# Kernel optimization log

Measured on AMD Instinct MI355X. Metric: run time of the kernel, lower is better.

## Reference

```python
import jax, jax.numpy as jnp
import numpy as np


def _three_nn(xyz1, xyz2):
    # xyz1: [B,N1,3], xyz2: [B,N2,3]
    # Squared euclidean distances, as in the original three_nn CUDA/TF op.
    d2 = (jnp.sum(xyz1 * xyz1, axis=-1)[:, :, None]
          + jnp.sum(xyz2 * xyz2, axis=-1)[:, None, :]
          - 2.0 * jnp.einsum('bnd,bmd->bnm', xyz1, xyz2))  # [B,N1,N2]
    neg_vals, idx = jax.lax.top_k(-d2, 3)                 # 3 smallest
    return -neg_vals, idx                                  # dist [B,N1,3], idx [B,N1,3]


def reference(xyz1, xyz2, points1, points2, w1, w2):
    dist, idx = _three_nn(xyz1, xyz2)
    dist = jnp.maximum(dist, 1e-10)
    inv = 1.0 / dist                                       # [B,N1,3]
    weight = inv / jnp.sum(inv, axis=2, keepdims=True)     # [B,N1,3]

    B = points2.shape[0]
    b_idx = jnp.arange(B)[:, None, None]
    gathered = points2[b_idx, idx]                         # [B,N1,3,C2]
    interpolated = jnp.einsum('bnk,bnkc->bnc', weight, gathered)  # [B,N1,C2]

    new_points = jnp.concatenate([interpolated, points1], axis=2)  # [B,N1,C2+C1]

    # 1x1 conv MLP = per-point matmul; bn=False, activation=relu on all layers
    h = jax.nn.relu(jnp.einsum('bnc,cf->bnf', new_points, w1))
    h = jax.nn.relu(jnp.einsum('bnc,cf->bnf', h, w2))
    return h


def setup_inputs() -> dict:
    key = jax.random.key(0)
    k1, k2, k3, k4, k5, k6 = jax.random.split(key, 6)
    B, N1, N2, C1, C2 = 4, 8192, 2048, 128, 256
    xyz1 = jax.random.normal(k1, (B, N1, 3), dtype=jnp.float32)
    xyz2 = jax.random.normal(k2, (B, N2, 3), dtype=jnp.float32)
    points1 = jax.random.normal(k3, (B, N1, C1), dtype=jnp.float32)
    points2 = jax.random.normal(k4, (B, N2, C2), dtype=jnp.float32)
    # glorot-normal-ish init for the 1x1 conv kernels
    w1 = jax.random.normal(k5, (C2 + C1, 256), dtype=jnp.float32) * (2.0 / (C2 + C1 + 256)) ** 0.5
    w2 = jax.random.normal(k6, (256, 256), dtype=jnp.float32) * (2.0 / (256 + 256)) ** 0.5
    return {"xyz1": xyz1, "xyz2": xyz2, "points1": points1, "points2": points2, "w1": w1, "w2": w2}
```

## Files before the change

### kernel.cpp

```cpp
#include <hip/hip_runtime.h>
#include <stdint.h>

typedef unsigned short u16;
typedef unsigned int   u32;

#define NB 4
#define N1 8192
#define N2 2048
#define C1 128
#define C2 256
#define KK1 384
#define FF 256
#define TM 64
#define NTHR 1024
#define NCH 16
#define PTSA 768
#define SUBA (PTSA / NCH)
#define PTSB 1280
#define SUBB (PTSB / NCH)
#define TILES_PER_B (N1 / TM)
#define APAD 400
#define HPAD 272
#define NKT1 (KK1 / 32)
#define NKT2 (FF / 32)

typedef short short8 __attribute__((ext_vector_type(8)));
typedef float floatx4 __attribute__((ext_vector_type(4)));
typedef float f32x2  __attribute__((ext_vector_type(2)));
typedef u32   u32x4  __attribute__((ext_vector_type(4)));

union ABFrag { u32 u[4]; short8 v; u32x4 q; };

__device__ __forceinline__ u16 f2b(float f) {
    u32 x = __float_as_uint(f);
    return (u16)((x + 0x7FFFu + ((x >> 16) & 1u)) >> 16);
}
__device__ __forceinline__ u32 pack2(float a, float b) {
    u32 r;
    asm("v_cvt_pk_bf16_f32 %0, %1, %2" : "=v"(r) : "v"(a), "v"(b));
    return r;
}

__global__ __launch_bounds__(256) void prep_kernel(
    const float* __restrict__ w1, const float* __restrict__ w2,
    const float* __restrict__ xyz2,
    u32x4* __restrict__ w1F, u32x4* __restrict__ w2F, float* __restrict__ xq)
{
    int i = blockIdx.x * 256 + threadIdx.x;
    if (i < 16 * NKT1 * 64) {
        int nt = i / (NKT1 * 64), rem = i % (NKT1 * 64);
        int kt = rem / 64, lane = rem % 64;
        int n  = nt * 16 + (lane & 15);
        int k0 = kt * 32 + (lane >> 4) * 8;
        const float* wc = w1 + n;
        ABFrag f;
        f.u[0] = pack2(wc[(k0 + 0) * FF], wc[(k0 + 1) * FF]);
        f.u[1] = pack2(wc[(k0 + 2) * FF], wc[(k0 + 3) * FF]);
        f.u[2] = pack2(wc[(k0 + 4) * FF], wc[(k0 + 5) * FF]);
        f.u[3] = pack2(wc[(k0 + 6) * FF], wc[(k0 + 7) * FF]);
        w1F[i] = f.q;
        return;
    }
    i -= 16 * NKT1 * 64;
    if (i < 16 * NKT2 * 64) {
        int nt = i / (NKT2 * 64), rem = i % (NKT2 * 64);
        int kt = rem / 64, lane = rem % 64;
        int n  = nt * 16 + (lane & 15);
        int k0 = kt * 32 + (lane >> 4) * 8;
        const float* wc = w2 + n;
        ABFrag f;
        f.u[0] = pack2(wc[(k0 + 0) * FF], wc[(k0 + 1) * FF]);
        f.u[1] = pack2(wc[(k0 + 2) * FF], wc[(k0 + 3) * FF]);
        f.u[2] = pack2(wc[(k0 + 4) * FF], wc[(k0 + 5) * FF]);
        f.u[3] = pack2(wc[(k0 + 6) * FF], wc[(k0 + 7) * FF]);
        w2F[i] = f.q;
        return;
    }
    i -= 16 * NKT2 * 64;
    if (i < NB * N2) {
        const float* q = xyz2 + (size_t)i * 3;
        float x = q[0], y = q[1], z = q[2];
        float s2 = __fadd_rn(__fadd_rn(__fmul_rn(x,x), __fmul_rn(y,y)), __fmul_rn(z,z));
        int p = i >> 1, e = i & 1;
        float* rec = xq + (size_t)p * 8;
        rec[0 + e] = -2.0f * x;
        rec[2 + e] = -2.0f * y;
        rec[4 + e] = -2.0f * z;
        rec[6 + e] = s2;
    }
}

__global__ __launch_bounds__(NTHR, 8) void fp_fused_kernel(
    const float* __restrict__ xyz1, const float* __restrict__ p1,
    const float* __restrict__ p2,
    const u32x4* __restrict__ w1F,  const u32x4* __restrict__ w2F,
    const float4* __restrict__ xq,  float* __restrict__ out)
{
    __shared__ int   s_idx[TM][3];
    __shared__ float s_wt[TM][3];
    __shared__ float s_m[TM][8];
    __shared__ float s_pd[NCH * TM * 3];
    __shared__ int   s_pi[NCH * TM * 3];
    __shared__ __align__(16) char s_buf[TM * APAD * 2];

    const int tid = threadIdx.x;
    const int b   = blockIdx.x / TILES_PER_B;
    const int t0  = (blockIdx.x % TILES_PER_B) * TM;
    u16* A = (u16*)s_buf;

    {
        const int c4 = (tid & 31) * 4, r32 = tid >> 5;
        #pragma unroll
        for (int rv = 0; rv < 2; ++rv) {
            int rr = r32 + rv * 32;
            float4 v = *(const float4*)(p1 + ((size_t)b * N1 + t0 + rr) * C1 + c4);
            u32* w = (u32*)(A + rr * APAD + 256 + c4);
            w[0] = pack2(v.x, v.y);
            w[1] = pack2(v.z, v.w);
        }
    }

    const int r  = tid & 63;
    const int ch = __builtin_amdgcn_readfirstlane(tid >> 6);

    const float* q = xyz1 + ((size_t)b * N1 + t0 + r) * 3;
    const float qx = q[0], qy = q[1], qz = q[2];
    const float s1 = __fadd_rn(__fadd_rn(__fmul_rn(qx,qx), __fmul_rn(qy,qy)), __fmul_rn(qz,qz));

    {
        const float4* cb = xq + ((size_t)b * (N2 / 2) + ch * (SUBA / 2)) * 2;
        float bd0 = 3e38f, bd1 = 3e38f, bd2 = 3e38f;
        int   bi0 = -1, bi1 = -1, bi2 = -1;
        const int j0 = ch * SUBA;
        #pragma unroll 8
        for (int jj = 0; jj < SUBA / 2; ++jj) {
            float4 f0 = cb[2 * jj];
            float4 f1 = cb[2 * jj + 1];
            f32x2 dpair;
            {
                #pragma clang fp contract(off)
                f32x2 qx2 = {qx, qx}, qy2 = {qy, qy}, qz2 = {qz, qz}, s1v = {s1, s1};
                f32x2 nx = {f0.x, f0.y}, ny = {f0.z, f0.w};
                f32x2 nz = {f1.x, f1.y}, ss = {f1.z, f1.w};
                f32x2 u  = qx2 * nx;
                f32x2 v  = qy2 * ny;
                f32x2 w  = u + v;
                f32x2 z2 = qz2 * nz;
                f32x2 t  = w + z2;
                f32x2 s12 = s1v + ss;
                dpair = s12 + t;
            }
            #pragma unroll
            for (int e = 0; e < 2; ++e) {
                float d = dpair[e];
                int   j = j0 + 2 * jj + e;
                float nb0 = fminf(d, bd0);
                float nb1 = __builtin_amdgcn_fmed3f(d, bd0, bd1);
                float nb2 = __builtin_amdgcn_fmed3f(d, bd1, bd2);
                bool c0 = d < bd0, c1 = d < bd1, c2 = d < bd2;
                int t01 = c0 ? bi0 : j;
                bi0     = c0 ? j   : bi0;
                int t12 = c1 ? bi1 : j;
                bi1     = c1 ? t01 : bi1;
                bi2     = c2 ? t12 : bi2;
                bd0 = nb0; bd1 = nb1; bd2 = nb2;
            }
        }
        const int o = (ch * TM + r) * 3;
        s_pd[o+0] = bd0; s_pd[o+1] = bd1; s_pd[o+2] = bd2;
        s_pi[o+0] = bi0; s_pi[o+1] = bi1; s_pi[o+2] = bi2;
    }
    __syncthreads();

    if (tid < TM) {
        float d0 = 3e38f, d1 = 3e38f, d2 = 3e38f;
        int   i0 = -1, i1 = -1, i2 = -1;
        for (int c = 0; c < NCH; ++c) {
            const int o = (c * TM + tid) * 3;
            #pragma unroll
            for (int k = 0; k < 3; ++k) {
                float d = s_pd[o + k]; int ix = s_pi[o + k];
                float n0 = fminf(d, d0);
                float n1 = __builtin_amdgcn_fmed3f(d, d0, d1);
                float n2 = __builtin_amdgcn_fmed3f(d, d1, d2);
                bool c0 = d < d0, c1 = d < d1, c2 = d < d2;
                int t01 = c0 ? i0 : ix;
                i0      = c0 ? ix : i0;
                int t12 = c1 ? i1 : t01;
                i1      = c1 ? t01 : i1;
                i2      = c2 ? t12 : i2;
                d0 = n0; d1 = n1; d2 = n2;
            }
        }
        s_m[tid][0] = d0; s_m[tid][1] = d1; s_m[tid][2] = d2;
        s_m[tid][4] = __int_as_float(i0);
        s_m[tid][5] = __int_as_float(i1);
        s_m[tid][6] = __int_as_float(i2);
    }
    __syncthreads();

    {
        const float bound = s_m[r][2];
        const float4* cb = xq + ((size_t)b * (N2 / 2) + (PTSA / 2) + ch * (SUBB / 2)) * 2;
        float bd0 = bound, bd1 = bound, bd2 = bound;
        int   bi0 = -1, bi1 = -1, bi2 = -1;
        const int j0 = PTSA + ch * SUBB;
        #pragma unroll 4
        for (int jj = 0; jj < SUBB / 2; ++jj) {
            float4 f0 = cb[2 * jj];
            float4 f1 = cb[2 * jj + 1];
            f32x2 dpair;
            {
                #pragma clang fp contract(off)
                f32x2 qx2 = {qx, qx}, qy2 = {qy, qy}, qz2 = {qz, qz}, s1v = {s1, s1};
                f32x2 nx = {f0.x, f0.y}, ny = {f0.z, f0.w};
                f32x2 nz = {f1.x, f1.y}, ss = {f1.z, f1.w};
                f32x2 u  = qx2 * nx;
                f32x2 v  = qy2 * ny;
                f32x2 w  = u + v;
                f32x2 z2 = qz2 * nz;
                f32x2 t  = w + z2;
                f32x2 s12 = s1v + ss;
                dpair = s12 + t;
            }
            if (__any((dpair.x < bd2) || (dpair.y < bd2))) {
                #pragma unroll
                for (int e = 0; e < 2; ++e) {
                    float d = dpair[e];
                    int   j = j0 + 2 * jj + e;
                    float nb0 = fminf(d, bd0);
                    float nb1 = __builtin_amdgcn_fmed3f(d, bd0, bd1);
                    float nb2 = __builtin_amdgcn_fmed3f(d, bd1, bd2);
                    bool c0 = d < bd0, c1 = d < bd1, c2 = d < bd2;
                    int t01 = c0 ? bi0 : j;
                    bi0     = c0 ? j   : bi0;
                    int t12 = c1 ? bi1 : j;
                    bi1     = c1 ? t01 : bi1;
                    bi2     = c2 ? t12 : bi2;
                    bd0 = nb0; bd1 = nb1; bd2 = nb2;
                }
            }
        }
        const int o = (ch * TM + r) * 3;
        s_pd[o+0] = bd0; s_pd[o+1] = bd1; s_pd[o+2] = bd2;
        s_pi[o+0] = bi0; s_pi[o+1] = bi1; s_pi[o+2] = bi2;
    }
    __syncthreads();

    if (tid < TM) {
        float d0 = s_m[tid][0], d1 = s_m[tid][1], d2 = s_m[tid][2];
        int   i0 = __float_as_int(s_m[tid][4]);
        int   i1 = __float_as_int(s_m[tid][5]);
        int   i2 = __float_as_int(s_m[tid][6]);
        for (int c = 0; c < NCH; ++c) {
            const int o = (c * TM + tid) * 3;
            #pragma unroll
            for (int k = 0; k < 3; ++k) {
                float d = s_pd[o + k]; int ix = s_pi[o + k];
                float n0 = fminf(d, d0);
                float n1 = __builtin_amdgcn_fmed3f(d, d0, d1);
                float n2 = __builtin_amdgcn_fmed3f(d, d1, d2);
                bool c0 = d < d0, c1 = d < d1, c2 = d < d2;
                int t01 = c0 ? i0 : ix;
                i0      = c0 ? ix : i0;
                int t12 = c1 ? i1 : t01;
                i1      = c1 ? t01 : i1;
                i2      = c2 ? t12 : i2;
                d0 = n0; d1 = n1; d2 = n2;
            }
        }
        d0 = fmaxf(d0, 1e-10f); d1 = fmaxf(d1, 1e-10f); d2 = fmaxf(d2, 1e-10f);
        float v0 = 1.0f / d0, v1 = 1.0f / d1, v2 = 1.0f / d2;
        float s  = 1.0f / (v0 + v1 + v2);
        s_wt[tid][0] = v0 * s; s_wt[tid][1] = v1 * s; s_wt[tid][2] = v2 * s;
        s_idx[tid][0] = i0; s_idx[tid][1] = i1; s_idx[tid][2] = i2;
    }
    __syncthreads();

    {
        const float* pb = p2 + (size_t)b * N2 * C2;
        const int col4 = (tid & 63) * 4;
        const int wvr  = tid >> 6;
        #pragma unroll
        for (int m = 0; m < 4; ++m) {
            int rr = wvr + m * 16;
            float w0 = s_wt[rr][0], w1v = s_wt[rr][1], w2v = s_wt[rr][2];
            int   i0 = s_idx[rr][0], i1 = s_idx[rr][1], i2 = s_idx[rr][2];
            float4 a0 = *(const float4*)(pb + (size_t)i0 * C2 + col4);
            float4 a1 = *(const float4*)(pb + (size_t)i1 * C2 + col4);
            float4 a2 = *(const float4*)(pb + (size_t)i2 * C2 + col4);
            float e0 = w0 * a0.x + w1v * a1.x + w2v * a2.x;
            float e1 = w0 * a0.y + w1v * a1.y + w2v * a2.y;
            float e2 = w0 * a0.z + w1v * a1.z + w2v * a2.z;
            float e3 = w0 * a0.w + w1v * a1.w + w2v * a2.w;
            u32* w = (u32*)(A + rr * APAD + col4);
            w[0] = pack2(e0, e1);
            w[1] = pack2(e2, e3);
        }
    }
    __syncthreads();

    const int lane = tid & 63;
    const int wv   = tid >> 6;
    const int lr   = lane & 15;
    const int lg   = lane >> 4;
    const int kb8  = lg * 8;
    const int wvb  = wv * 16;

    int id1[4], id2[4];
    {
        u16 rbf = f2b((float)lr);
        u16 c32 = f2b(1.0f / 32.0f);
        ABFrag pa, pc;
        u32 ra = (u32)rbf | ((u32)rbf << 16);
        u32 rc = (u32)c32 | ((u32)c32 << 16);
        pa.u[0] = pa.u[1] = pa.u[2] = pa.u[3] = ra;
        pc.u[0] = pc.u[1] = pc.u[2] = pc.u[3] = rc;
        floatx4 z = {0.f, 0.f, 0.f, 0.f};
        floatx4 D1 = __builtin_amdgcn_mfma_f32_16x16x32_bf16(pa.v, pc.v, z, 0, 0, 0);
        floatx4 D2 = __builtin_amdgcn_mfma_f32_16x16x32_bf16(pc.v, pa.v, z, 0, 0, 0);
        #pragma unroll
        for (int g = 0; g < 4; ++g) { id1[g] = (int)(D1[g] + 0.5f); id2[g] = (int)(D2[g] + 0.5f); }
    }

    floatx4 acc[4];
    #pragma unroll
    for (int i = 0; i < 4; ++i) acc[i] = floatx4{0.f, 0.f, 0.f, 0.f};
    {
        const u32x4* wf = w1F + (size_t)(wv * NKT1) * 64 + lane;
        #pragma unroll 2
        for (int kk = 0; kk < NKT1; ++kk) {
            ABFrag bf; bf.q = wf[(size_t)kk * 64];
            ABFrag a[4];
            #pragma unroll
            for (int rt = 0; rt < 4; ++rt)
                a[rt].q = *(const u32x4*)(A + (rt * 16 + lr) * APAD + kk * 32 + kb8);
            #pragma unroll
            for (int rt = 0; rt < 4; ++rt)
                acc[rt] = __builtin_amdgcn_mfma_f32_16x16x32_bf16(a[rt].v, bf.v, acc[rt], 0, 0, 0);
        }
    }
    __syncthreads();

    u16* H = (u16*)s_buf;
    #pragma unroll
    for (int rt = 0; rt < 4; ++rt)
        #pragma unroll
        for (int g = 0; g < 4; ++g) {
            int row = rt * 16 + id1[g];
            int col = wvb + id2[g];
            H[row * HPAD + col] = f2b(fmaxf(acc[rt][g], 0.0f));
        }
    __syncthreads();

    floatx4 acc2[4];
    #pragma unroll
    for (int i = 0; i < 4; ++i) acc2[i] = floatx4{0.f, 0.f, 0.f, 0.f};
    {
        const u32x4* wf = w2F + (size_t)(wv * NKT2) * 64 + lane;
        #pragma unroll 2
        for (int kk = 0; kk < NKT2; ++kk) {
            ABFrag bf; bf.q = wf[(size_t)kk * 64];
            ABFrag a[4];
            #pragma unroll
            for (int rt = 0; rt < 4; ++rt)
                a[rt].q = *(const u32x4*)(H + (rt * 16 + lr) * HPAD + kk * 32 + kb8);
            #pragma unroll
            for (int rt = 0; rt < 4; ++rt)
                acc2[rt] = __builtin_amdgcn_mfma_f32_16x16x32_bf16(a[rt].v, bf.v, acc2[rt], 0, 0, 0);
        }
    }

    float* ob = out + ((size_t)b * N1 + t0) * FF;
    #pragma unroll
    for (int rt = 0; rt < 4; ++rt)
        #pragma unroll
        for (int g = 0; g < 4; ++g) {
            int row = rt * 16 + id1[g];
            int col = wvb + id2[g];
            ob[(size_t)row * FF + col] = fmaxf(acc2[rt][g], 0.0f);
        }
}

extern "C" void kernel_launch(void* const* d_in, const int* in_sizes, int n_in,
                              void* d_out, int out_size, void* d_ws, size_t ws_size,
                              hipStream_t stream)
{
    (void)in_sizes; (void)n_in; (void)out_size; (void)ws_size;
    const float* xyz1 = (const float*)d_in[0];
    const float* xyz2 = (const float*)d_in[1];
    const float* p1   = (const float*)d_in[2];
    const float* p2   = (const float*)d_in[3];
    const float* w1   = (const float*)d_in[4];
    const float* w2   = (const float*)d_in[5];
    float* out = (float*)d_out;

    u32x4* w1F = (u32x4*)d_ws;
    u32x4* w2F = w1F + 16 * NKT1 * 64;
    float* xqw = (float*)(w2F + 16 * NKT2 * 64);

    int prep_items = 16 * NKT1 * 64 + 16 * NKT2 * 64 + NB * N2;
    prep_kernel<<<(prep_items + 255) / 256, 256, 0, stream>>>(w1, w2, xyz2, w1F, w2F, xqw);
    fp_fused_kernel<<<NB * TILES_PER_B, NTHR, 0, stream>>>(
        xyz1, p1, p2, w1F, w2F, (const float4*)xqw, out);
}
```

Measured before the change: 59.56 us.

## Parallelize top-3 chunk merges and prefetch gathers and weight fragments

The 16-chunk top-3 merge done by 64 threads is split into two levels: 256 threads first merge groups of 4 chunks into scratch shared memory, then 64 threads merge the 4 partials. This shortens the serial merge phases. The points1 tile load is issued before the NN scan and written to LDS afterward, which hides its global latency. The gather of points2 rows is double-buffered across rows, and the MFMA loops prefetch the next weight fragment. In exchange the kernel gains an extra barrier per merge stage and uses more registers for the prefetched values.

Result: faster. 57.75 us (-3.0%).

```diff
diff --git a/kernel.cpp b/kernel.cpp
--- a/kernel.cpp
+++ b/kernel.cpp
@@ -41,6 +41,20 @@
     return r;
 }
 
+#define INS3(d, ix, d0, d1, d2, i0, i1, i2)                         \
+    {                                                               \
+        float n0 = fminf(d, d0);                                    \
+        float n1 = __builtin_amdgcn_fmed3f(d, d0, d1);              \
+        float n2 = __builtin_amdgcn_fmed3f(d, d1, d2);              \
+        bool c0 = d < d0, c1 = d < d1, c2 = d < d2;                 \
+        int t01 = c0 ? i0 : ix;                                     \
+        i0      = c0 ? ix : i0;                                     \
+        int t12 = c1 ? i1 : t01;                                    \
+        i1      = c1 ? t01 : i1;                                    \
+        i2      = c2 ? t12 : i2;                                    \
+        d0 = n0; d1 = n1; d2 = n2;                                  \
+    }
+
 __global__ __launch_bounds__(256) void prep_kernel(
     const float* __restrict__ w1, const float* __restrict__ w2,
     const float* __restrict__ xyz2,
@@ -108,17 +122,9 @@
     const int t0  = (blockIdx.x % TILES_PER_B) * TM;
     u16* A = (u16*)s_buf;
 
-    {
-        const int c4 = (tid & 31) * 4, r32 = tid >> 5;
-        #pragma unroll
-        for (int rv = 0; rv < 2; ++rv) {
-            int rr = r32 + rv * 32;
-            float4 v = *(const float4*)(p1 + ((size_t)b * N1 + t0 + rr) * C1 + c4);
-            u32* w = (u32*)(A + rr * APAD + 256 + c4);
-            w[0] = pack2(v.x, v.y);
-            w[1] = pack2(v.z, v.w);
-        }
-    }
+    const int c4 = (tid & 31) * 4, r32 = tid >> 5;
+    float4 pv0 = *(const float4*)(p1 + ((size_t)b * N1 + t0 + r32) * C1 + c4);
+    float4 pv1 = *(const float4*)(p1 + ((size_t)b * N1 + t0 + r32 + 32) * C1 + c4);
 
     const int r  = tid & 63;
     const int ch = __builtin_amdgcn_readfirstlane(tid >> 6);
@@ -154,42 +160,53 @@
             for (int e = 0; e < 2; ++e) {
                 float d = dpair[e];
                 int   j = j0 + 2 * jj + e;
-                float nb0 = fminf(d, bd0);
-                float nb1 = __builtin_amdgcn_fmed3f(d, bd0, bd1);
-                float nb2 = __builtin_amdgcn_fmed3f(d, bd1, bd2);
-                bool c0 = d < bd0, c1 = d < bd1, c2 = d < bd2;
-                int t01 = c0 ? bi0 : j;
-                bi0     = c0 ? j   : bi0;
-                int t12 = c1 ? bi1 : j;
-                bi1     = c1 ? t01 : bi1;
-                bi2     = c2 ? t12 : bi2;
-                bd0 = nb0; bd1 = nb1; bd2 = nb2;
+                INS3(d, j, bd0, bd1, bd2, bi0, bi1, bi2);
             }
         }
         const int o = (ch * TM + r) * 3;
         s_pd[o+0] = bd0; s_pd[o+1] = bd1; s_pd[o+2] = bd2;
         s_pi[o+0] = bi0; s_pi[o+1] = bi1; s_pi[o+2] = bi2;
     }
+
+    {
+        u32* w0 = (u32*)(A + r32 * APAD + 256 + c4);
+        w0[0] = pack2(pv0.x, pv0.y);
+        w0[1] = pack2(pv0.z, pv0.w);
+        u32* w1p = (u32*)(A + (r32 + 32) * APAD + 256 + c4);
+        w1p[0] = pack2(pv1.x, pv1.y);
+        w1p[1] = pack2(pv1.z, pv1.w);
+    }
+    __syncthreads();
+
+    if (tid < 256) {
+        const int row = tid & 63, grp = tid >> 6;
+        float d0 = 3e38f, d1 = 3e38f, d2 = 3e38f;
+        int   i0 = -1, i1 = -1, i2 = -1;
+        #pragma unroll
+        for (int c = 0; c < 4; ++c) {
+            const int o = ((grp * 4 + c) * TM + row) * 3;
+            #pragma unroll
+            for (int k = 0; k < 3; ++k) {
+                float d = s_pd[o + k]; int ix = s_pi[o + k];
+                INS3(d, ix, d0, d1, d2, i0, i1, i2);
+            }
+        }
+        float* sg = (float*)(s_buf + row * (APAD * 2) + grp * 32);
+        sg[0] = d0; sg[1] = d1; sg[2] = d2;
+        sg[3] = __int_as_float(i0); sg[4] = __int_as_float(i1); sg[5] = __int_as_float(i2);
+    }
     __syncthreads();
 
     if (tid < TM) {
         float d0 = 3e38f, d1 = 3e38f, d2 = 3e38f;
         int   i0 = -1, i1 = -1, i2 = -1;
-        for (int c = 0; c < NCH; ++c) {
-            const int o = (c * TM + tid) * 3;
+        #pragma unroll
+        for (int g = 0; g < 4; ++g) {
+            const float* sg = (const float*)(s_buf + tid * (APAD * 2) + g * 32);
             #pragma unroll
             for (int k = 0; k < 3; ++k) {
-                float d = s_pd[o + k]; int ix = s_pi[o + k];
-                float n0 = fminf(d, d0);
-                float n1 = __builtin_amdgcn_fmed3f(d, d0, d1);
-                float n2 = __builtin_amdgcn_fmed3f(d, d1, d2);
-                bool c0 = d < d0, c1 = d < d1, c2 = d < d2;
-                int t01 = c0 ? i0 : ix;
-                i0      = c0 ? ix : i0;
-                int t12 = c1 ? i1 : t01;
-                i1      = c1 ? t01 : i1;
-                i2      = c2 ? t12 : i2;
-                d0 = n0; d1 = n1; d2 = n2;
+                float d = sg[k]; int ix = __float_as_int(sg[3 + k]);
+                INS3(d, ix, d0, d1, d2, i0, i1, i2);
             }
         }
         s_m[tid][0] = d0; s_m[tid][1] = d1; s_m[tid][2] = d2;
@@ -228,22 +245,32 @@
                 for (int e = 0; e < 2; ++e) {
                     float d = dpair[e];
                     int   j = j0 + 2 * jj + e;
-                    float nb0 = fminf(d, bd0);
-                    float nb1 = __builtin_amdgcn_fmed3f(d, bd0, bd1);
-                    float nb2 = __builtin_amdgcn_fmed3f(d, bd1, bd2);
-                    bool c0 = d < bd0, c1 = d < bd1, c2 = d < bd2;
-                    int t01 = c0 ? bi0 : j;
-                    bi0     = c0 ? j   : bi0;
-                    int t12 = c1 ? bi1 : j;
-                    bi1     = c1 ? t01 : bi1;
-                    bi2     = c2 ? t12 : bi2;
-                    bd0 = nb0; bd1 = nb1; bd2 = nb2;
+                    INS3(d, j, bd0, bd1, bd2, bi0, bi1, bi2);
                 }
             }
         }
         const int o = (ch * TM + r) * 3;
         s_pd[o+0] = bd0; s_pd[o+1] = bd1; s_pd[o+2] = bd2;
         s_pi[o+0] = bi0; s_pi[o+1] = bi1; s_pi[o+2] = bi2;
+    }
+    __syncthreads();
+
+    if (tid < 256) {
+        const int row = tid & 63, grp = tid >> 6;
+        float d0 = 3e38f, d1 = 3e38f, d2 = 3e38f;
+        int   i0 = -1, i1 = -1, i2 = -1;
+        #pragma unroll
+        for (int c = 0; c < 4; ++c) {
+            const int o = ((grp * 4 + c) * TM + row) * 3;
+            #pragma unroll
+            for (int k = 0; k < 3; ++k) {
+                float d = s_pd[o + k]; int ix = s_pi[o + k];
+                INS3(d, ix, d0, d1, d2, i0, i1, i2);
+            }
+        }
+        float* sg = (float*)(s_buf + row * (APAD * 2) + grp * 32);
+        sg[0] = d0; sg[1] = d1; sg[2] = d2;
+        sg[3] = __int_as_float(i0); sg[4] = __int_as_float(i1); sg[5] = __int_as_float(i2);
     }
     __syncthreads();
 
@@ -252,21 +279,13 @@
         int   i0 = __float_as_int(s_m[tid][4]);
         int   i1 = __float_as_int(s_m[tid][5]);
         int   i2 = __float_as_int(s_m[tid][6]);
-        for (int c = 0; c < NCH; ++c) {
-            const int o = (c * TM + tid) * 3;
+        #pragma unroll
+        for (int g = 0; g < 4; ++g) {
+            const float* sg = (const float*)(s_buf + tid * (APAD * 2) + g * 32);
             #pragma unroll
             for (int k = 0; k < 3; ++k) {
-                float d = s_pd[o + k]; int ix = s_pi[o + k];
-                float n0 = fminf(d, d0);
-                float n1 = __builtin_amdgcn_fmed3f(d, d0, d1);
-                float n2 = __builtin_amdgcn_fmed3f(d, d1, d2);
-                bool c0 = d < d0, c1 = d < d1, c2 = d < d2;
-                int t01 = c0 ? i0 : ix;
-                i0      = c0 ? ix : i0;
-                int t12 = c1 ? i1 : t01;
-                i1      = c1 ? t01 : i1;
-                i2      = c2 ? t12 : i2;
-                d0 = n0; d1 = n1; d2 = n2;
+                float d = sg[k]; int ix = __float_as_int(sg[3 + k]);
+                INS3(d, ix, d0, d1, d2, i0, i1, i2);
             }
         }
         d0 = fmaxf(d0, 1e-10f); d1 = fmaxf(d1, 1e-10f); d2 = fmaxf(d2, 1e-10f);
@@ -281,18 +300,28 @@
         const float* pb = p2 + (size_t)b * N2 * C2;
         const int col4 = (tid & 63) * 4;
         const int wvr  = tid >> 6;
+        float4 a0[2], a1[2], a2[2];
+        {
+            int rr = wvr;
+            a0[0] = *(const float4*)(pb + (size_t)s_idx[rr][0] * C2 + col4);
+            a1[0] = *(const float4*)(pb + (size_t)s_idx[rr][1] * C2 + col4);
+            a2[0] = *(const float4*)(pb + (size_t)s_idx[rr][2] * C2 + col4);
+        }
         #pragma unroll
         for (int m = 0; m < 4; ++m) {
+            int cur = m & 1, nxt = cur ^ 1;
+            if (m < 3) {
+                int rn = wvr + (m + 1) * 16;
+                a0[nxt] = *(const float4*)(pb + (size_t)s_idx[rn][0] * C2 + col4);
+                a1[nxt] = *(const float4*)(pb + (size_t)s_idx[rn][1] * C2 + col4);
+                a2[nxt] = *(const float4*)(pb + (size_t)s_idx[rn][2] * C2 + col4);
+            }
             int rr = wvr + m * 16;
             float w0 = s_wt[rr][0], w1v = s_wt[rr][1], w2v = s_wt[rr][2];
-            int   i0 = s_idx[rr][0], i1 = s_idx[rr][1], i2 = s_idx[rr][2];
-            float4 a0 = *(const float4*)(pb + (size_t)i0 * C2 + col4);
-            float4 a1 = *(const float4*)(pb + (size_t)i1 * C2 + col4);
-            float4 a2 = *(const float4*)(pb + (size_t)i2 * C2 + col4);
-            float e0 = w0 * a0.x + w1v * a1.x + w2v * a2.x;
-            float e1 = w0 * a0.y + w1v * a1.y + w2v * a2.y;
-            float e2 = w0 * a0.z + w1v * a1.z + w2v * a2.z;
-            float e3 = w0 * a0.w + w1v * a1.w + w2v * a2.w;
+            float e0 = w0 * a0[cur].x + w1v * a1[cur].x + w2v * a2[cur].x;
+            float e1 = w0 * a0[cur].y + w1v * a1[cur].y + w2v * a2[cur].y;
+            float e2 = w0 * a0[cur].z + w1v * a1[cur].z + w2v * a2[cur].z;
+            float e3 = w0 * a0[cur].w + w1v * a1[cur].w + w2v * a2[cur].w;
             u32* w = (u32*)(A + rr * APAD + col4);
             w[0] = pack2(e0, e1);
             w[1] = pack2(e2, e3);
@@ -328,16 +357,19 @@
     for (int i = 0; i < 4; ++i) acc[i] = floatx4{0.f, 0.f, 0.f, 0.f};
     {
         const u32x4* wf = w1F + (size_t)(wv * NKT1) * 64 + lane;
+        ABFrag bfc; bfc.q = wf[0];
         #pragma unroll 2
         for (int kk = 0; kk < NKT1; ++kk) {
-            ABFrag bf; bf.q = wf[(size_t)kk * 64];
+            ABFrag bfn;
+            bfn.q = wf[(size_t)((kk + 1 < NKT1) ? kk + 1 : kk) * 64];
             ABFrag a[4];
             #pragma unroll
             for (int rt = 0; rt < 4; ++rt)
                 a[rt].q = *(const u32x4*)(A + (rt * 16 + lr) * APAD + kk * 32 + kb8);
             #pragma unroll
             for (int rt = 0; rt < 4; ++rt)
-                acc[rt] = __builtin_amdgcn_mfma_f32_16x16x32_bf16(a[rt].v, bf.v, acc[rt], 0, 0, 0);
+                acc[rt] = __builtin_amdgcn_mfma_f32_16x16x32_bf16(a[rt].v, bfc.v, acc[rt], 0, 0, 0);
+            bfc = bfn;
         }
     }
     __syncthreads();
@@ -358,16 +390,19 @@
     for (int i = 0; i < 4; ++i) acc2[i] = floatx4{0.f, 0.f, 0.f, 0.f};
     {
         const u32x4* wf = w2F + (size_t)(wv * NKT2) * 64 + lane;
+        ABFrag bfc; bfc.q = wf[0];
         #pragma unroll 2
         for (int kk = 0; kk < NKT2; ++kk) {
-            ABFrag bf; bf.q = wf[(size_t)kk * 64];
+            ABFrag bfn;
+            bfn.q = wf[(size_t)((kk + 1 < NKT2) ? kk + 1 : kk) * 64];
             ABFrag a[4];
             #pragma unroll
             for (int rt = 0; rt < 4; ++rt)
                 a[rt].q = *(const u32x4*)(H + (rt * 16 + lr) * HPAD + kk * 32 + kb8);
             #pragma unroll
             for (int rt = 0; rt < 4; ++rt)
-                acc2[rt] = __builtin_amdgcn_mfma_f32_16x16x32_bf16(a[rt].v, bf.v, acc2[rt], 0, 0, 0);
+                acc2[rt] = __builtin_amdgcn_mfma_f32_16x16x32_bf16(a[rt].v, bfc.v, acc2[rt], 0, 0, 0);
+            bfc = bfn;
         }
     }
 
```
